# Kernel tuning notes

Hardware: AMD Instinct MI355X
Metric: run time of the kernel (lower is better)

The kernel has to match this reference:

```python
import jax, jax.numpy as jnp
import numpy as np

# GDN (gated delta-rule) linear attention, prefill path, single packed sequence,
# no initial conv/ssm state.
NUM_K_HEADS = 16
NUM_V_HEADS = 32
HEAD_K_DIM = 128
HEAD_V_DIM = 128
HIDDEN = 2048
CONV_K = 4
EPS = 1e-6
K_TOTAL = NUM_K_HEADS * HEAD_K_DIM
V_TOTAL = NUM_V_HEADS * HEAD_V_DIM
QKV_TOTAL = 2 * K_TOTAL + V_TOTAL


def setup_inputs() -> dict:
    key = jax.random.key(0)
    ks = jax.random.split(key, 9)
    T = 2048
    s = 0.02
    return {
        "hidden_states": jax.random.normal(ks[0], (T, HIDDEN), jnp.float32),
        "in_proj_qkv_weight": s * jax.random.normal(ks[1], (QKV_TOTAL, HIDDEN), jnp.float32),
        "in_proj_z_weight": s * jax.random.normal(ks[2], (V_TOTAL, HIDDEN), jnp.float32),
        "in_proj_a_weight": s * jax.random.normal(ks[3], (NUM_V_HEADS, HIDDEN), jnp.float32),
        "in_proj_b_weight": s * jax.random.normal(ks[4], (NUM_V_HEADS, HIDDEN), jnp.float32),
        "conv1d_weight": 0.1 * jax.random.normal(ks[5], (QKV_TOTAL, CONV_K), jnp.float32),
        "out_proj_weight": s * jax.random.normal(ks[6], (HIDDEN, V_TOTAL), jnp.float32),
        "norm_weight": jnp.ones((HEAD_V_DIM,), jnp.float32),
        "A_log": jnp.log(jnp.linspace(1.0, 8.0, NUM_V_HEADS, dtype=jnp.float32)),
        "dt_bias": 0.5 * jax.random.normal(ks[7], (NUM_V_HEADS,), jnp.float32),
    }


def _causal_conv1d_silu(x, w):
    # x: [T, C], w: [C, K] depthwise causal conv + SiLU
    T = x.shape[0]
    K = w.shape[1]
    xp = jnp.pad(x, ((K - 1, 0), (0, 0)))
    y = xp[0:T] * w[:, 0]
    for j in range(1, K):  # small fixed K
        y = y + xp[j:j + T] * w[:, j]
    return jax.nn.silu(y)


def _l2norm(x):
    return x / jnp.sqrt(jnp.sum(x * x, axis=-1, keepdims=True) + EPS)


def _gdn_recurrence(q, k, v, g, beta, scale):
    # q,k: [T,Hv,Dk] (l2-normed, repeated over GQA groups), v: [T,Hv,Dv]
    # g,beta: [T,Hv]. State S: [Hv,Dk,Dv]. Gated delta rule:
    #   S <- exp(g)*S ; S <- S + k^T beta (v - k S) ; o = scale * q S
    Hv, Dk = q.shape[1], q.shape[2]
    Dv = v.shape[2]

    def step(S, inp):
        q_t, k_t, v_t, g_t, b_t = inp
        S = S * jnp.exp(g_t)[:, None, None]
        pred = jnp.einsum('hk,hkv->hv', k_t, S)
        delta = b_t[:, None] * (v_t - pred)
        S = S + jnp.einsum('hk,hv->hkv', k_t, delta)
        o = jnp.einsum('hk,hkv->hv', q_t * scale, S)
        return S, o

    S0 = jnp.zeros((Hv, Dk, Dv), q.dtype)
    _, o = jax.lax.scan(step, S0, (q, k, v, g, beta))
    return o  # [T,Hv,Dv]


def reference(hidden_states, in_proj_qkv_weight, in_proj_z_weight, in_proj_a_weight,
              in_proj_b_weight, conv1d_weight, out_proj_weight, norm_weight, A_log, dt_bias):
    T = hidden_states.shape[0]
    mixed = hidden_states @ in_proj_qkv_weight.T            # [T, QKV_TOTAL]
    z = hidden_states @ in_proj_z_weight.T                  # [T, V_TOTAL]
    a = hidden_states @ in_proj_a_weight.T                  # [T, Hv]
    b = hidden_states @ in_proj_b_weight.T                  # [T, Hv]

    mixed = _causal_conv1d_silu(mixed, conv1d_weight)

    q, k, v = jnp.split(mixed, [K_TOTAL, 2 * K_TOTAL], axis=-1)
    q = q.reshape(T, NUM_K_HEADS, HEAD_K_DIM)
    k = k.reshape(T, NUM_K_HEADS, HEAD_K_DIM)
    v = v.reshape(T, NUM_V_HEADS, HEAD_V_DIM)

    # qk l2-norm in kernel, GQA repeat to v heads
    q = _l2norm(q)
    k = _l2norm(k)
    ratio = NUM_V_HEADS // NUM_K_HEADS
    q = jnp.repeat(q, ratio, axis=1)
    k = jnp.repeat(k, ratio, axis=1)

    # fused_gdn_gating: g = -exp(A_log) * softplus(a + dt_bias); beta = sigmoid(b)
    g = -jnp.exp(A_log) * jax.nn.softplus(a + dt_bias)      # [T,Hv]
    beta = jax.nn.sigmoid(b)                                # [T,Hv]

    o = _gdn_recurrence(q, k, v, g, beta, HEAD_K_DIM ** -0.5)  # [T,Hv,Dv]

    # gated RMSNorm: rmsnorm(o) * norm_weight * silu(z)
    o = o * jax.lax.rsqrt(jnp.mean(o * o, axis=-1, keepdims=True) + EPS) * norm_weight
    o = o * jax.nn.silu(z.reshape(T, NUM_V_HEADS, HEAD_V_DIM))

    return o.reshape(T, -1) @ out_proj_weight.T             # [T, HIDDEN]
```

## Files before the change

### kernel.cpp

```cpp
#include <hip/hip_runtime.h>
#include <math.h>

#define T_SEQ     2048
#define HIDDEN_D  2048
#define NUM_KH    16
#define NUM_VH    32
#define HEAD_DIM  128
#define K_TOTAL   2048
#define V_TOTAL   4096
#define QKV_TOTAL 8192
#define EPS_F     1e-6f
#define CC        32
#define NCHUNK    (T_SEQ / CC)
#define NV        8

typedef __attribute__((ext_vector_type(4))) float f32x4;
typedef __attribute__((ext_vector_type(8))) short s16x8;
typedef __attribute__((ext_vector_type(8))) unsigned short u16x8;

__device__ __forceinline__ unsigned short f2bf(float f) {
    unsigned int u = __float_as_uint(f);
    u += 0x7FFFu + ((u >> 16) & 1u);
    return (unsigned short)(u >> 16);
}

__device__ __forceinline__ float bf2f(unsigned short h) {
    return __uint_as_float((unsigned int)h << 16);
}

__global__ __launch_bounds__(256) void cast_bf16_kernel(
    const float* __restrict__ src, unsigned short* __restrict__ dst, int n4)
{
    int idx = blockIdx.x * 256 + threadIdx.x;
    if (idx >= n4) return;
    float4 v = ((const float4*)src)[idx];
    ushort4 o;
    o.x = f2bf(v.x); o.y = f2bf(v.y); o.z = f2bf(v.z); o.w = f2bf(v.w);
    ((ushort4*)dst)[idx] = o;
}

__global__ __launch_bounds__(256) void gemm_bt_bf16(
    const unsigned short* __restrict__ A, const unsigned short* __restrict__ B,
    float* __restrict__ C, int M, int N, int K)
{
    __shared__ unsigned short As[128 * 64];
    __shared__ unsigned short Bs[128 * 64];
    const int tid  = threadIdx.x;
    const int wave = tid >> 6;
    const int lane = tid & 63;
    const int m0 = blockIdx.y * 128;
    const int n0 = blockIdx.x * 128;
    const int wm = (wave >> 1) * 64;
    const int wn = (wave & 1) * 64;

    f32x4 acc[4][4];
    f32x4 zero = {0.f, 0.f, 0.f, 0.f};
#pragma unroll
    for (int i = 0; i < 4; ++i)
#pragma unroll
        for (int j = 0; j < 4; ++j) acc[i][j] = zero;

    const int srow = lane >> 3;
    const int scol = (lane & 7) * 8;
    const int rm = lane & 15;
    const int koq = (lane >> 4) * 8;

    for (int kt = 0; kt < K; kt += 64) {
#pragma unroll
        for (int l = 0; l < 4; ++l) {
            const int r0 = wave * 32 + l * 8;
            const unsigned short* ga =
                A + (size_t)(m0 + r0 + srow) * K + kt + scol;
            const unsigned short* gb =
                B + (size_t)(n0 + r0 + srow) * K + kt + scol;
            __builtin_amdgcn_global_load_lds(
                (const __attribute__((address_space(1))) void*)ga,
                (__attribute__((address_space(3))) void*)&As[r0 * 64], 16, 0, 0);
            __builtin_amdgcn_global_load_lds(
                (const __attribute__((address_space(1))) void*)gb,
                (__attribute__((address_space(3))) void*)&Bs[r0 * 64], 16, 0, 0);
        }
        __syncthreads();

#pragma unroll
        for (int ks = 0; ks < 2; ++ks) {
            const int ko = ks * 32 + koq;
            s16x8 af[4], bfr[4];
#pragma unroll
            for (int i = 0; i < 4; ++i) {
                af[i]  = *(const s16x8*)&As[(wm + i * 16 + rm) * 64 + ko];
                bfr[i] = *(const s16x8*)&Bs[(wn + i * 16 + rm) * 64 + ko];
            }
#pragma unroll
            for (int i = 0; i < 4; ++i)
#pragma unroll
                for (int j = 0; j < 4; ++j)
                    acc[i][j] = __builtin_amdgcn_mfma_f32_16x16x32_bf16(
                        af[i], bfr[j], acc[i][j], 0, 0, 0);
        }
        __syncthreads();
    }

    const int cr = (lane >> 4) * 4;
    const int ccol = lane & 15;
#pragma unroll
    for (int i = 0; i < 4; ++i)
#pragma unroll
        for (int j = 0; j < 4; ++j) {
#pragma unroll
            for (int r = 0; r < 4; ++r)
                C[(size_t)(m0 + wm + i * 16 + cr + r) * N
                  + n0 + wn + j * 16 + ccol] = acc[i][j][r];
        }
}

__global__ __launch_bounds__(256) void gemm_nt_64(
    const float* __restrict__ A, const float* __restrict__ B,
    float* __restrict__ C, int M, int N, int K)
{
    __shared__ float As[16][68];
    __shared__ float Bs[16][68];
    const int tid = threadIdx.x;
    const int m0 = blockIdx.y * 64;
    const int n0 = blockIdx.x * 64;
    const int tm = tid >> 4;
    const int tn = tid & 15;
    const int lr = tid >> 2;
    const int lc = (tid & 3) * 4;

    float acc[4][4];
#pragma unroll
    for (int i = 0; i < 4; ++i)
#pragma unroll
        for (int j = 0; j < 4; ++j) acc[i][j] = 0.f;

    for (int kt = 0; kt < K; kt += 16) {
        float4 av = *(const float4*)(A + (size_t)(m0 + lr) * K + kt + lc);
        float4 bv = *(const float4*)(B + (size_t)(n0 + lr) * K + kt + lc);
        As[lc + 0][lr] = av.x; As[lc + 1][lr] = av.y;
        As[lc + 2][lr] = av.z; As[lc + 3][lr] = av.w;
        Bs[lc + 0][lr] = bv.x; Bs[lc + 1][lr] = bv.y;
        Bs[lc + 2][lr] = bv.z; Bs[lc + 3][lr] = bv.w;
        __syncthreads();
#pragma unroll
        for (int kk = 0; kk < 16; ++kk) {
            float4 a4 = *(const float4*)&As[kk][tm * 4];
            float4 b4 = *(const float4*)&Bs[kk][tn * 4];
            float a[4] = {a4.x, a4.y, a4.z, a4.w};
            float b[4] = {b4.x, b4.y, b4.z, b4.w};
#pragma unroll
            for (int i = 0; i < 4; ++i)
#pragma unroll
                for (int j = 0; j < 4; ++j)
                    acc[i][j] = fmaf(a[i], b[j], acc[i][j]);
        }
        __syncthreads();
    }
#pragma unroll
    for (int i = 0; i < 4; ++i) {
        float4 o = make_float4(acc[i][0], acc[i][1], acc[i][2], acc[i][3]);
        *(float4*)(C + (size_t)(m0 + tm * 4 + i) * N + n0 + tn * 4) = o;
    }
}

__global__ __launch_bounds__(256) void concat_ab_kernel(
    const float* __restrict__ Wa, const float* __restrict__ Wb,
    float* __restrict__ Wab)
{
    int idx = blockIdx.x * 256 + threadIdx.x;
    int half = 16384;
    const float* src = (idx < half) ? Wa : Wb;
    int off = (idx < half) ? idx : idx - half;
    ((float4*)Wab)[idx] = ((const float4*)src)[off];
}

__global__ __launch_bounds__(256) void gating_finalize_kernel(
    const float* __restrict__ ab, const float* __restrict__ A_log,
    const float* __restrict__ dt_bias, float* __restrict__ g,
    float* __restrict__ beta)
{
    int idx = blockIdx.x * 256 + threadIdx.x;
    int t = idx >> 5, h = idx & 31;
    float a = ab[t * 64 + h] + dt_bias[h];
    float b = ab[t * 64 + 32 + h];
    float sp = (a > 20.f) ? a : log1pf(expf(a));
    g[idx] = -expf(A_log[h]) * sp;
    beta[idx] = 1.f / (1.f + expf(-b));
}

__global__ __launch_bounds__(256) void conv_silu_kernel(
    const float* __restrict__ mixed, const float* __restrict__ cw,
    float* __restrict__ qkv)
{
    int idx = blockIdx.x * 256 + threadIdx.x;
    int c = idx & (QKV_TOTAL - 1);
    int t = idx >> 13;
    const float4 w = *(const float4*)(cw + (size_t)c * 4);
    float y = w.w * mixed[(size_t)t * QKV_TOTAL + c];
    if (t >= 1) y = fmaf(w.z, mixed[(size_t)(t - 1) * QKV_TOTAL + c], y);
    if (t >= 2) y = fmaf(w.y, mixed[(size_t)(t - 2) * QKV_TOTAL + c], y);
    if (t >= 3) y = fmaf(w.x, mixed[(size_t)(t - 3) * QKV_TOTAL + c], y);
    qkv[(size_t)t * QKV_TOTAL + c] = y / (1.f + expf(-y));
}

__global__ __launch_bounds__(64) void l2norm_kernel(float* __restrict__ qkv)
{
    const int row = blockIdx.x;
    const int t = row >> 5;
    const int r = row & 31;
    float* p = qkv + (size_t)t * QKV_TOTAL + r * HEAD_DIM;
    const int lane = threadIdx.x;
    float2 v = *(float2*)(p + lane * 2);
    float s = v.x * v.x + v.y * v.y;
    for (int off = 32; off > 0; off >>= 1) s += __shfl_down(s, off);
    s = __shfl(s, 0);
    float inv = rsqrtf(s + EPS_F);
    v.x *= inv; v.y *= inv;
    *(float2*)(p + lane * 2) = v;
}

__global__ __launch_bounds__(256) void gdn_p1(
    const float* __restrict__ qkv, const float* __restrict__ g,
    const float* __restrict__ beta, float* __restrict__ PTbuf,
    unsigned short* __restrict__ K2buf, float* __restrict__ lam_g,
    float* __restrict__ bet_g)
{
    __shared__ float Kn[CC][132];
    __shared__ float Qn[CC][132];
    __shared__ float Wm[CC][33];
    __shared__ float Tld[CC][36];
    __shared__ float Pm[CC][33];
    __shared__ float Trl[CC][33];
    __shared__ float cums[CC];
    __shared__ float betas[CC];
    __shared__ float rlS[CC];

    const int tid = threadIdx.x;
    const int h   = blockIdx.x;
    const int cix = blockIdx.y;
    const int t0  = cix * CC;
    const int kh  = h >> 1;
    const float scale = 0.08838834764831845f;
    const size_t mb = ((size_t)cix * NUM_VH + h);
    const size_t sb = mb * CC;

    if (tid < CC) {
        float x = g[(size_t)(t0 + tid) * NUM_VH + h];
        float bv = beta[(size_t)(t0 + tid) * NUM_VH + h];
#pragma unroll
        for (int off = 1; off < 32; off <<= 1) {
            float n = __shfl_up(x, off);
            if (tid >= off) x += n;
        }
        cums[tid] = x;
        betas[tid] = bv;
        float c31 = __shfl(x, 31);
        lam_g[sb + tid] = expf(x);
        bet_g[sb + tid] = bv;
        rlS[tid] = expf(c31 - x);
    }
#pragma unroll
    for (int p = 0; p < 4; ++p) {
        int idx = p * 256 + tid;
        int i = idx >> 5, k4 = (idx & 31) * 4;
        const float* qr = qkv + (size_t)(t0 + i) * QKV_TOTAL + kh * HEAD_DIM + k4;
        float4 q4 = *(const float4*)qr;
        float4 k4v = *(const float4*)(qr + K_TOTAL);
        *(float4*)&Kn[i][k4] = k4v;
        q4.x *= scale; q4.y *= scale; q4.z *= scale; q4.w *= scale;
        *(float4*)&Qn[i][k4] = q4;
    }
    __syncthreads();

    {
        const int i0 = (tid >> 4) * 2, j0 = (tid & 15) * 2;
        float wa[2][2] = {{0.f, 0.f}, {0.f, 0.f}};
        float pa[2][2] = {{0.f, 0.f}, {0.f, 0.f}};
        for (int k = 0; k < HEAD_DIM; k += 4) {
            float4 a0 = *(const float4*)&Kn[i0][k];
            float4 a1 = *(const float4*)&Kn[i0 + 1][k];
            float4 b0 = *(const float4*)&Kn[j0][k];
            float4 b1 = *(const float4*)&Kn[j0 + 1][k];
            float4 c0 = *(const float4*)&Qn[i0][k];
            float4 c1 = *(const float4*)&Qn[i0 + 1][k];
            const float* ap0 = (const float*)&a0;
            const float* ap1 = (const float*)&a1;
            const float* bp0 = (const float*)&b0;
            const float* bp1 = (const float*)&b1;
            const float* cp0 = (const float*)&c0;
            const float* cp1 = (const float*)&c1;
#pragma unroll
            for (int cc = 0; cc < 4; ++cc) {
                wa[0][0] = fmaf(ap0[cc], bp0[cc], wa[0][0]);
                wa[0][1] = fmaf(ap0[cc], bp1[cc], wa[0][1]);
                wa[1][0] = fmaf(ap1[cc], bp0[cc], wa[1][0]);
                wa[1][1] = fmaf(ap1[cc], bp1[cc], wa[1][1]);
                pa[0][0] = fmaf(cp0[cc], bp0[cc], pa[0][0]);
                pa[0][1] = fmaf(cp0[cc], bp1[cc], pa[0][1]);
                pa[1][0] = fmaf(cp1[cc], bp0[cc], pa[1][0]);
                pa[1][1] = fmaf(cp1[cc], bp1[cc], pa[1][1]);
            }
        }
#pragma unroll
        for (int di = 0; di < 2; ++di)
#pragma unroll
            for (int dj = 0; dj < 2; ++dj) {
                int i = i0 + di, j = j0 + dj;
                float rr = expf(fminf(cums[i] - cums[j], 0.f));
                Wm[i][j] = (j < i) ? betas[i] * rr * wa[di][dj] : 0.f;
                Pm[i][j] = (j <= i) ? rr * pa[di][dj] : 0.f;
            }
    }
    __syncthreads();

    {
        const int col = tid >> 3, tk = tid & 7;
        if (tk == 0) Tld[0][col] = (col == 0) ? 1.f : 0.f;
        for (int i = 1; i < CC; ++i) {
            float part = 0.f;
            for (int j = tk; j < i; j += 8)
                part = fmaf(Wm[i][j], Tld[j][col], part);
            part += __shfl_xor(part, 4);
            part += __shfl_xor(part, 2);
            part += __shfl_xor(part, 1);
            if (tk == 0) Tld[i][col] = ((i == col) ? 1.f : 0.f) - part;
        }
    }
    __syncthreads();

    {
        const int i = tid >> 3, j0 = (tid & 7) * 4;
        const float r = rlS[i];
#pragma unroll
        for (int e = 0; e < 4; ++e)
            Trl[i][j0 + e] = Tld[i][j0 + e] * r;
        float4 accp = {0.f, 0.f, 0.f, 0.f};
        for (int m = 0; m < CC; ++m) {
            float pv = Pm[i][m];
            float4 tv = *(const float4*)&Tld[m][j0];
            accp.x = fmaf(pv, tv.x, accp.x);
            accp.y = fmaf(pv, tv.y, accp.y);
            accp.z = fmaf(pv, tv.z, accp.z);
            accp.w = fmaf(pv, tv.w, accp.w);
        }
        *(float4*)(PTbuf + mb * (CC * CC) + tid * 4) = accp;
    }
    __syncthreads();

    {
        const int m0 = tid >> 3;
        const int q  = (tid & 7) * 4;
        float acc[4][4];
#pragma unroll
        for (int c = 0; c < 4; ++c)
#pragma unroll
            for (int e = 0; e < 4; ++e) acc[c][e] = 0.f;
        for (int j = 0; j < CC; ++j) {
            float t = Trl[j][m0];
#pragma unroll
            for (int c = 0; c < 4; ++c) {
                float4 a = *(const float4*)&Kn[j][q + 32 * c];
                acc[c][0] = fmaf(t, a.x, acc[c][0]);
                acc[c][1] = fmaf(t, a.y, acc[c][1]);
                acc[c][2] = fmaf(t, a.z, acc[c][2]);
                acc[c][3] = fmaf(t, a.w, acc[c][3]);
            }
        }
        unsigned short* kout =
            K2buf + mb * (CC * HEAD_DIM) + m0 * HEAD_DIM + q;
#pragma unroll
        for (int c = 0; c < 4; ++c) {
            ushort4 o4;
            o4.x = f2bf(acc[c][0]); o4.y = f2bf(acc[c][1]);
            o4.z = f2bf(acc[c][2]); o4.w = f2bf(acc[c][3]);
            *(ushort4*)(kout + 32 * c) = o4;
        }
    }
}

__global__ __launch_bounds__(256) void gdn_p2(
    const float* __restrict__ qkv, const float* __restrict__ PTbuf,
    const unsigned short* __restrict__ K2buf, const float* __restrict__ lam_g,
    const float* __restrict__ bet_g, float* __restrict__ o)
{
    __shared__ float Kn[CC][132];
    __shared__ float Qn[CC][132];
    __shared__ unsigned short K2l[CC][136];
    __shared__ float PTl[CC][36];
    __shared__ float Sm[HEAD_DIM][NV + 2];
    __shared__ float Dl[CC][NV + 2];
    __shared__ float lamS[CC], betS[CC];

    const int tid = threadIdx.x;
    const int h   = blockIdx.x >> 4;
    const int V0  = (blockIdx.x & 15) * NV;
    const int kh  = h >> 1;
    const float scale = 0.08838834764831845f;

    const int ri = tid >> 3;
    const int rn = (tid & 3) * 2;
    const int hh = (tid >> 2) & 1;
    const int kb = hh * 64;

    const int fk = (tid >> 3) * 4;
    const int sn = tid & 7;

#pragma unroll
    for (int c = 0; c < 4; ++c) Sm[fk + c][sn] = 0.f;

    for (int cix = 0; cix < NCHUNK; ++cix) {
        const int t0 = cix * CC;
        const size_t mb = ((size_t)cix * NUM_VH + h);
        __syncthreads();

#pragma unroll
        for (int p = 0; p < 4; ++p) {
            int idx = p * 256 + tid;
            int i = idx >> 5, k4 = (idx & 31) * 4;
            const float* qr = qkv + (size_t)(t0 + i) * QKV_TOTAL + kh * HEAD_DIM + k4;
            float4 q4 = *(const float4*)qr;
            float4 k4v = *(const float4*)(qr + K_TOTAL);
            *(float4*)&Kn[i][k4] = k4v;
            q4.x *= scale; q4.y *= scale; q4.z *= scale; q4.w *= scale;
            *(float4*)&Qn[i][k4] = q4;
        }
#pragma unroll
        for (int p = 0; p < 2; ++p) {
            int idx = p * 256 + tid;
            int i = idx >> 4, k8 = (idx & 15) * 8;
            *(u16x8*)&K2l[i][k8] =
                *(const u16x8*)(K2buf + mb * (CC * HEAD_DIM) + i * HEAD_DIM + k8);
        }
        {
            float4 t4 = *(const float4*)(PTbuf + mb * (CC * CC) + tid * 4);
            *(float4*)&PTl[tid >> 3][(tid & 7) * 4] = t4;
        }
        if (tid < CC) {
            lamS[tid] = lam_g[mb * CC + tid];
            betS[tid] = bet_g[mb * CC + tid];
        }
        float2 v2 = *(const float2*)(qkv + (size_t)(t0 + ri) * QKV_TOTAL
                                     + 2 * K_TOTAL + h * HEAD_DIM + V0 + rn);
        __syncthreads();

        float r1x = 0.f, r1y = 0.f, r2x = 0.f, r2y = 0.f;
        for (int k = 0; k < 64; k += 4) {
            float4 kv = *(const float4*)&Kn[ri][kb + k];
            float4 qv = *(const float4*)&Qn[ri][kb + k];
            const float* kp = (const float*)&kv;
            const float* qp = (const float*)&qv;
#pragma unroll
            for (int c4 = 0; c4 < 4; ++c4) {
                float2 s = *(const float2*)&Sm[kb + k + c4][rn];
                r1x = fmaf(kp[c4], s.x, r1x);
                r1y = fmaf(kp[c4], s.y, r1y);
                r2x = fmaf(qp[c4], s.x, r2x);
                r2y = fmaf(qp[c4], s.y, r2y);
            }
        }
        r1x += __shfl_xor(r1x, 4);
        r1y += __shfl_xor(r1y, 4);
        r2x += __shfl_xor(r2x, 4);
        r2y += __shfl_xor(r2y, 4);
        {
            float lam = lamS[ri], bet = betS[ri];
            float dlx = bet * (v2.x - lam * r1x);
            float dly = bet * (v2.y - lam * r1y);
            r2x *= lam; r2y *= lam;
            if (hh == 0) { Dl[ri][rn] = dlx; Dl[ri][rn + 1] = dly; }
        }
        __syncthreads();

        {
            float ox = r2x, oy = r2y;
            for (int j = 0; j < CC; ++j) {
                float p = PTl[ri][j];
                float2 d = *(const float2*)&Dl[j][rn];
                ox = fmaf(p, d.x, ox);
                oy = fmaf(p, d.y, oy);
            }
            if (hh == 0)
                *(float2*)(o + (size_t)(t0 + ri) * V_TOTAL + h * HEAD_DIM + V0 + rn)
                    = make_float2(ox, oy);
        }

        {
            const float lamL = lamS[CC - 1];
            float s0 = lamL * Sm[fk + 0][sn];
            float s1 = lamL * Sm[fk + 1][sn];
            float s2 = lamL * Sm[fk + 2][sn];
            float s3 = lamL * Sm[fk + 3][sn];
            for (int j = 0; j < CC; ++j) {
                ushort4 kk = *(const ushort4*)&K2l[j][fk];
                float d = Dl[j][sn];
                s0 = fmaf(bf2f(kk.x), d, s0);
                s1 = fmaf(bf2f(kk.y), d, s1);
                s2 = fmaf(bf2f(kk.z), d, s2);
                s3 = fmaf(bf2f(kk.w), d, s3);
            }
            Sm[fk + 0][sn] = s0;
            Sm[fk + 1][sn] = s1;
            Sm[fk + 2][sn] = s2;
            Sm[fk + 3][sn] = s3;
        }
    }
}

__global__ __launch_bounds__(64) void rmsnorm_gate_kernel(
    float* __restrict__ o, const float* __restrict__ z,
    const float* __restrict__ nw)
{
    const int row = blockIdx.x;
    float* p = o + (size_t)row * HEAD_DIM;
    const float* zp = z + (size_t)row * HEAD_DIM;
    const int lane = threadIdx.x;
    float2 v = *(float2*)(p + lane * 2);
    float s = v.x * v.x + v.y * v.y;
    for (int off = 32; off > 0; off >>= 1) s += __shfl_down(s, off);
    s = __shfl(s, 0);
    float inv = rsqrtf(s * (1.f / HEAD_DIM) + EPS_F);
    float2 zv = *(float2*)(zp + lane * 2);
    float2 wv = *(const float2*)(nw + lane * 2);
    v.x = v.x * inv * wv.x * (zv.x / (1.f + expf(-zv.x)));
    v.y = v.y * inv * wv.y * (zv.y / (1.f + expf(-zv.y)));
    *(float2*)(p + lane * 2) = v;
}

extern "C" void kernel_launch(void* const* d_in, const int* in_sizes, int n_in,
                              void* d_out, int out_size, void* d_ws,
                              size_t ws_size, hipStream_t stream)
{
    const float* hs    = (const float*)d_in[0];
    const float* Wqkv  = (const float*)d_in[1];
    const float* Wz    = (const float*)d_in[2];
    const float* Wa    = (const float*)d_in[3];
    const float* Wb    = (const float*)d_in[4];
    const float* cw    = (const float*)d_in[5];
    const float* Wout  = (const float*)d_in[6];
    const float* nw    = (const float*)d_in[7];
    const float* A_log = (const float*)d_in[8];
    const float* dtb   = (const float*)d_in[9];
    float* out = (float*)d_out;

    float* F     = (float*)d_ws;
    float* mixed = F;
    float* qkvb  = F + (size_t)16777216;
    float* zb    = F + (size_t)33554432;
    float* gb    = F + (size_t)41943040;
    float* bb    = F + (size_t)42008576;
    float* ob    = mixed;

    float* PTbuf = F + (size_t)8388608;
    unsigned short* K2buf = (unsigned short*)(F + (size_t)10485760);
    float* lam_b = F + (size_t)14680064;
    float* bet_b = F + (size_t)14745600;

    unsigned short* hs_bf   = (unsigned short*)(F + (size_t)16777216);
    unsigned short* Wqkv_bf = (unsigned short*)(F + (size_t)18874368);
    unsigned short* Wz_bf   = (unsigned short*)(F + (size_t)27262976);
    unsigned short* ob_bf   = (unsigned short*)(F + (size_t)33554432);
    unsigned short* Wout_bf = (unsigned short*)(F + (size_t)37748736);

    float* Wab = F + (size_t)27262976;
    float* ab  = F + (size_t)27394048;

    cast_bf16_kernel<<<1048576 / 256, 256, 0, stream>>>(hs, hs_bf, 1048576);
    cast_bf16_kernel<<<4194304 / 256, 256, 0, stream>>>(Wqkv, Wqkv_bf, 4194304);
    cast_bf16_kernel<<<2097152 / 256, 256, 0, stream>>>(Wz, Wz_bf, 2097152);
    gemm_bt_bf16<<<dim3(QKV_TOTAL / 128, T_SEQ / 128), 256, 0, stream>>>(
        hs_bf, Wqkv_bf, mixed, T_SEQ, QKV_TOTAL, HIDDEN_D);
    gemm_bt_bf16<<<dim3(V_TOTAL / 128, T_SEQ / 128), 256, 0, stream>>>(
        hs_bf, Wz_bf, zb, T_SEQ, V_TOTAL, HIDDEN_D);
    concat_ab_kernel<<<32768 / 256, 256, 0, stream>>>(Wa, Wb, Wab);
    gemm_nt_64<<<dim3(1, T_SEQ / 64), 256, 0, stream>>>(
        hs, Wab, ab, T_SEQ, 64, HIDDEN_D);
    gating_finalize_kernel<<<(T_SEQ * NUM_VH) / 256, 256, 0, stream>>>(
        ab, A_log, dtb, gb, bb);
    conv_silu_kernel<<<(T_SEQ * QKV_TOTAL) / 256, 256, 0, stream>>>(
        mixed, cw, qkvb);
    l2norm_kernel<<<T_SEQ * 32, 64, 0, stream>>>(qkvb);
    gdn_p1<<<dim3(NUM_VH, NCHUNK), 256, 0, stream>>>(
        qkvb, gb, bb, PTbuf, K2buf, lam_b, bet_b);
    gdn_p2<<<NUM_VH * (HEAD_DIM / NV), 256, 0, stream>>>(
        qkvb, PTbuf, K2buf, lam_b, bet_b, ob);
    rmsnorm_gate_kernel<<<T_SEQ * NUM_VH, 64, 0, stream>>>(ob, zb, nw);
    cast_bf16_kernel<<<2097152 / 256, 256, 0, stream>>>(ob, ob_bf, 2097152);
    cast_bf16_kernel<<<2097152 / 256, 256, 0, stream>>>(Wout, Wout_bf, 2097152);
    gemm_bt_bf16<<<dim3(HIDDEN_D / 128, T_SEQ / 128), 256, 0, stream>>>(
        ob_bf, Wout_bf, out, T_SEQ, HIDDEN_D, V_TOTAL);
}
```

Measured before the change: 1.031 ms.

## Double-buffer GDN chunk loads with async global-to-LDS DMA and swizzled layout

Restructures the chunked recurrence kernel so the next chunk's K/Q, K2, PT, lambda/beta and V are prefetched while the current chunk's output and state-update phases run. K/Q and K2 now go straight to shared memory through global_load_lds, with K2, PT and the gate values double-buffered. The K/Q shared layout drops its padding and uses an XOR swizzle to avoid bank conflicts. The q scale is moved from the loaded data to the output. Correctness relies on the async LDS writes being finished by the next barrier, and the extra buffers use more shared memory.

Result: slower. 1.056 ms (+2.4%).

```diff
diff --git a/kernel.cpp b/kernel.cpp
--- a/kernel.cpp
+++ b/kernel.cpp
@@ -16,7 +16,6 @@
 
 typedef __attribute__((ext_vector_type(4))) float f32x4;
 typedef __attribute__((ext_vector_type(8))) short s16x8;
-typedef __attribute__((ext_vector_type(8))) unsigned short u16x8;
 
 __device__ __forceinline__ unsigned short f2bf(float f) {
     unsigned int u = __float_as_uint(f);
@@ -383,15 +382,17 @@
     const unsigned short* __restrict__ K2buf, const float* __restrict__ lam_g,
     const float* __restrict__ bet_g, float* __restrict__ o)
 {
-    __shared__ float Kn[CC][132];
-    __shared__ float Qn[CC][132];
-    __shared__ unsigned short K2l[CC][136];
-    __shared__ float PTl[CC][36];
+    __shared__ float Kn[CC][128];
+    __shared__ float Qn[CC][128];
+    __shared__ unsigned short K2l[2][CC][128];
+    __shared__ float PTl[2][CC][36];
     __shared__ float Sm[HEAD_DIM][NV + 2];
     __shared__ float Dl[CC][NV + 2];
-    __shared__ float lamS[CC], betS[CC];
+    __shared__ float lamS[2][CC], betS[2][CC];
 
     const int tid = threadIdx.x;
+    const int wv  = tid >> 6;
+    const int ln  = tid & 63;
     const int h   = blockIdx.x >> 4;
     const int V0  = (blockIdx.x & 15) * NV;
     const int kh  = h >> 1;
@@ -400,58 +401,82 @@
     const int ri = tid >> 3;
     const int rn = (tid & 3) * 2;
     const int hh = (tid >> 2) & 1;
-    const int kb = hh * 64;
+    const int hh4 = hh * 4;
+    const int rx = ri & 3;
 
     const int fk = (tid >> 3) * 4;
     const int sn = tid & 7;
 
+    const int drow = wv * 2 + (ln >> 5);
+    const int dw   = ln & 31;
+
+#define DMA_KQ(T0)                                                            \
+    {                                                                         \
+        _Pragma("unroll")                                                     \
+        for (int p = 0; p < 4; ++p) {                                         \
+            const int i = p * 8 + drow;                                       \
+            const int u = dw ^ ((i & 3) << 1);                                \
+            const float* sq = qkv + (size_t)((T0) + i) * QKV_TOTAL            \
+                              + kh * HEAD_DIM + u * 4;                        \
+            __builtin_amdgcn_global_load_lds(                                 \
+                (const __attribute__((address_space(1))) void*)(sq + K_TOTAL),\
+                (__attribute__((address_space(3))) void*)                     \
+                    &Kn[p * 8 + wv * 2][0], 16, 0, 0);                        \
+            __builtin_amdgcn_global_load_lds(                                 \
+                (const __attribute__((address_space(1))) void*)sq,            \
+                (__attribute__((address_space(3))) void*)                     \
+                    &Qn[p * 8 + wv * 2][0], 16, 0, 0);                        \
+        }                                                                     \
+    }
+
+#define DMA_K2(MB, BUF)                                                       \
+    {                                                                         \
+        _Pragma("unroll")                                                     \
+        for (int p = 0; p < 2; ++p) {                                         \
+            const unsigned short* sk = K2buf + (MB) * (CC * HEAD_DIM)         \
+                                       + p * 2048 + wv * 512 + ln * 8;        \
+            __builtin_amdgcn_global_load_lds(                                 \
+                (const __attribute__((address_space(1))) void*)sk,            \
+                (__attribute__((address_space(3))) void*)                     \
+                    &K2l[BUF][p * 16 + wv * 4][0], 16, 0, 0);                 \
+        }                                                                     \
+    }
+
 #pragma unroll
     for (int c = 0; c < 4; ++c) Sm[fk + c][sn] = 0.f;
 
+    DMA_KQ(0);
+    DMA_K2((size_t)h, 0);
+    {
+        float4 pt0 = *(const float4*)(PTbuf + (size_t)h * (CC * CC) + tid * 4);
+        *(float4*)&PTl[0][tid >> 3][(tid & 7) * 4] = pt0;
+        if (tid < CC) {
+            lamS[0][tid] = lam_g[(size_t)h * CC + tid];
+            betS[0][tid] = bet_g[(size_t)h * CC + tid];
+        }
+    }
+    float2 vR = *(const float2*)(qkv + (size_t)ri * QKV_TOTAL
+                                 + 2 * K_TOTAL + h * HEAD_DIM + V0 + rn);
+
+    int cur = 0;
     for (int cix = 0; cix < NCHUNK; ++cix) {
         const int t0 = cix * CC;
-        const size_t mb = ((size_t)cix * NUM_VH + h);
         __syncthreads();
 
-#pragma unroll
-        for (int p = 0; p < 4; ++p) {
-            int idx = p * 256 + tid;
-            int i = idx >> 5, k4 = (idx & 31) * 4;
-            const float* qr = qkv + (size_t)(t0 + i) * QKV_TOTAL + kh * HEAD_DIM + k4;
-            float4 q4 = *(const float4*)qr;
-            float4 k4v = *(const float4*)(qr + K_TOTAL);
-            *(float4*)&Kn[i][k4] = k4v;
-            q4.x *= scale; q4.y *= scale; q4.z *= scale; q4.w *= scale;
-            *(float4*)&Qn[i][k4] = q4;
-        }
-#pragma unroll
-        for (int p = 0; p < 2; ++p) {
-            int idx = p * 256 + tid;
-            int i = idx >> 4, k8 = (idx & 15) * 8;
-            *(u16x8*)&K2l[i][k8] =
-                *(const u16x8*)(K2buf + mb * (CC * HEAD_DIM) + i * HEAD_DIM + k8);
-        }
-        {
-            float4 t4 = *(const float4*)(PTbuf + mb * (CC * CC) + tid * 4);
-            *(float4*)&PTl[tid >> 3][(tid & 7) * 4] = t4;
-        }
-        if (tid < CC) {
-            lamS[tid] = lam_g[mb * CC + tid];
-            betS[tid] = bet_g[mb * CC + tid];
-        }
-        float2 v2 = *(const float2*)(qkv + (size_t)(t0 + ri) * QKV_TOTAL
-                                     + 2 * K_TOTAL + h * HEAD_DIM + V0 + rn);
-        __syncthreads();
-
+        const float lam = lamS[cur][ri];
+        const float bet = betS[cur][ri];
         float r1x = 0.f, r1y = 0.f, r2x = 0.f, r2y = 0.f;
-        for (int k = 0; k < 64; k += 4) {
-            float4 kv = *(const float4*)&Kn[ri][kb + k];
-            float4 qv = *(const float4*)&Qn[ri][kb + k];
+#pragma unroll
+        for (int kk = 0; kk < 16; ++kk) {
+            const int cp = ((kk ^ rx) << 3) + hh4;
+            const int cl = (kk << 3) + hh4;
+            float4 kv = *(const float4*)&Kn[ri][cp];
+            float4 qv = *(const float4*)&Qn[ri][cp];
             const float* kp = (const float*)&kv;
             const float* qp = (const float*)&qv;
 #pragma unroll
             for (int c4 = 0; c4 < 4; ++c4) {
-                float2 s = *(const float2*)&Sm[kb + k + c4][rn];
+                float2 s = *(const float2*)&Sm[cl + c4][rn];
                 r1x = fmaf(kp[c4], s.x, r1x);
                 r1y = fmaf(kp[c4], s.y, r1y);
                 r2x = fmaf(qp[c4], s.x, r2x);
@@ -463,18 +488,34 @@
         r2x += __shfl_xor(r2x, 4);
         r2y += __shfl_xor(r2y, 4);
         {
-            float lam = lamS[ri], bet = betS[ri];
-            float dlx = bet * (v2.x - lam * r1x);
-            float dly = bet * (v2.y - lam * r1y);
-            r2x *= lam; r2y *= lam;
+            float dlx = bet * (vR.x - lam * r1x);
+            float dly = bet * (vR.y - lam * r1y);
             if (hh == 0) { Dl[ri][rn] = dlx; Dl[ri][rn + 1] = dly; }
         }
+        const float lsc = lam * scale;
+        float ox = r2x * lsc, oy = r2y * lsc;
         __syncthreads();
 
+        const int nxt = cur ^ 1;
+        float4 ptN; float lamN = 0.f, betN = 0.f; float2 vN;
+        const int more = (cix + 1 < NCHUNK);
+        if (more) {
+            const int t0n = t0 + CC;
+            const size_t mbn = (size_t)(cix + 1) * NUM_VH + h;
+            DMA_KQ(t0n);
+            DMA_K2(mbn, nxt);
+            ptN = *(const float4*)(PTbuf + mbn * (CC * CC) + tid * 4);
+            if (tid < CC) {
+                lamN = lam_g[mbn * CC + tid];
+                betN = bet_g[mbn * CC + tid];
+            }
+            vN = *(const float2*)(qkv + (size_t)(t0n + ri) * QKV_TOTAL
+                                  + 2 * K_TOTAL + h * HEAD_DIM + V0 + rn);
+        }
+
         {
-            float ox = r2x, oy = r2y;
             for (int j = 0; j < CC; ++j) {
-                float p = PTl[ri][j];
+                float p = PTl[cur][ri][j];
                 float2 d = *(const float2*)&Dl[j][rn];
                 ox = fmaf(p, d.x, ox);
                 oy = fmaf(p, d.y, oy);
@@ -485,13 +526,13 @@
         }
 
         {
-            const float lamL = lamS[CC - 1];
+            const float lamL = lamS[cur][CC - 1];
             float s0 = lamL * Sm[fk + 0][sn];
             float s1 = lamL * Sm[fk + 1][sn];
             float s2 = lamL * Sm[fk + 2][sn];
             float s3 = lamL * Sm[fk + 3][sn];
             for (int j = 0; j < CC; ++j) {
-                ushort4 kk = *(const ushort4*)&K2l[j][fk];
+                ushort4 kk = *(const ushort4*)&K2l[cur][j][fk];
                 float d = Dl[j][sn];
                 s0 = fmaf(bf2f(kk.x), d, s0);
                 s1 = fmaf(bf2f(kk.y), d, s1);
@@ -503,7 +544,16 @@
             Sm[fk + 2][sn] = s2;
             Sm[fk + 3][sn] = s3;
         }
-    }
+
+        if (more) {
+            *(float4*)&PTl[nxt][tid >> 3][(tid & 7) * 4] = ptN;
+            if (tid < CC) { lamS[nxt][tid] = lamN; betS[nxt][tid] = betN; }
+            vR = vN;
+        }
+        cur = nxt;
+    }
+#undef DMA_KQ
+#undef DMA_K2
 }
 
 __global__ __launch_bounds__(64) void rmsnorm_gate_kernel(
```
